# Kernel optimization log

Hardware: AMD Instinct MI355X
Metric: run time of the kernel (lower is better)

The kernel has to match this reference:

```python
import jax, jax.numpy as jnp
import numpy as np

PAD = 3            # pad_size
K = 3              # kernel_size
MAX_DISP = 20      # max_displacement
STRIDE1 = 1
STRIDE2 = 2

B, C, H, W = 4, 128, 192, 192


def _correlation(input1, input2):
    """FlowNetC/PWC-Net correlation cost volume (correlation_pwc semantics).

    input1, input2: [B, C, H, W]
    returns: [B, D*D, Hout, Wout] where D = 2*(MAX_DISP//STRIDE2)+1.
    """
    b, c, h, w = input1.shape
    kr = (K - 1) // 2                      # kernel radius
    br = kr + MAX_DISP                     # border radius
    hp, wp = h + 2 * PAD, w + 2 * PAD      # padded sizes
    hout = (hp - 2 * br) // STRIDE1
    wout = (wp - 2 * br) // STRIDE1
    gr = MAX_DISP // STRIDE2               # neighborhood grid radius
    disp = jnp.arange(-gr, gr + 1, dtype=jnp.int32) * STRIDE2
    # channel order: tj (dy) outer, ti (dx) inner, matching the CUDA kernel
    dyx = jnp.stack(jnp.meshgrid(disp, disp, indexing='ij'), axis=-1).reshape(-1, 2)

    pad1 = jnp.pad(input1, ((0, 0), (0, 0), (PAD, PAD), (PAD, PAD)))
    pad2 = jnp.pad(input2, ((0, 0), (0, 0), (PAD, PAD), (PAD, PAD)))

    # region of pad1 touched by all outputs (stride1 == 1)
    hh, ww = hout * STRIDE1 + 2 * kr, wout * STRIDE1 + 2 * kr
    s1 = pad1[:, :, MAX_DISP:MAX_DISP + hh, MAX_DISP:MAX_DISP + ww]
    nelems = K * K * c

    def step(_, d):
        dy, dx = d[0], d[1]
        s2 = jax.lax.dynamic_slice(pad2, (0, 0, MAX_DISP + dy, MAX_DISP + dx),
                                   (b, c, hh, ww))
        prod = jnp.sum(s1 * s2, axis=1)  # [B, hh, ww] reduce channels
        summed = jax.lax.reduce_window(prod, 0.0, jax.lax.add,
                                       (1, K, K), (1, STRIDE1, STRIDE1), 'VALID')
        return None, summed / nelems      # [B, Hout, Wout]

    _, out = jax.lax.scan(step, None, dyx)   # [D*D, B, Hout, Wout]
    return jnp.transpose(out, (1, 0, 2, 3))  # [B, D*D, Hout, Wout]


def setup_inputs() -> dict:
    key = jax.random.key(0)
    k1, k2 = jax.random.split(key)
    input1 = jax.random.normal(k1, (B, C, H, W), dtype=jnp.float32)
    input2 = jax.random.normal(k2, (B, C, H, W), dtype=jnp.float32)
    return {"input1": input1, "input2": input2}


def reference(input1, input2):
    return _correlation(input1, input2)
```

## Files before the change

### kernel.cpp

```cpp
#include <hip/hip_runtime.h>
#include <hip/hip_bf16.h>


#define C_    128
#define H_    192
#define W_    192
#define HW_   36864
#define NE_   18874368
#define CORR_E 44036496
#define WS_NEED 163570464ull

typedef __attribute__((ext_vector_type(8))) short short8;
typedef __attribute__((ext_vector_type(4))) float floatx4;

__device__ __forceinline__ float bf2f(ushort h) {
    uint u = ((uint)h) << 16;
    return __builtin_bit_cast(float, u);
}
__device__ __forceinline__ ushort f2bf(float f) {
    __hip_bfloat16 hb = __float2bfloat16(f);
    return *(ushort*)&hb;
}

__global__ __launch_bounds__(256)
void cvt_t_kernel(const float* __restrict__ a, const float* __restrict__ b,
                  ushort* __restrict__ dst0) {
    __shared__ float tile[128 * 65];
    const float* src = blockIdx.z ? b : a;
    ushort* dst = dst0 + (size_t)blockIdx.z * NE_;
    const int bb = blockIdx.y;
    const int hw0 = blockIdx.x * 64;
    const int t = threadIdx.x;
    const int xr = (t & 15) * 4;
    const int c0 = t >> 4;
    const float* sbase = src + (size_t)bb * C_ * HW_ + hw0;
#pragma unroll
    for (int pass = 0; pass < 8; ++pass) {
        const int c = c0 + 16 * pass;
        float4 v = *(const float4*)(sbase + (size_t)c * HW_ + xr);
        float* lp = &tile[c * 65 + xr];
        lp[0] = v.x; lp[1] = v.y; lp[2] = v.z; lp[3] = v.w;
    }
    __syncthreads();
    ushort* obase = dst + ((size_t)bb * HW_ + hw0) * 128;
#pragma unroll
    for (int pass = 0; pass < 4; ++pass) {
        const int u = t + 256 * pass;
        const int x = u >> 4, oc = u & 15;
        uint w[4];
#pragma unroll
        for (int k = 0; k < 4; ++k) {
            const float f0 = tile[(oc * 8 + 2 * k) * 65 + x];
            const float f1 = tile[(oc * 8 + 2 * k + 1) * 65 + x];
            w[k] = (uint)f2bf(f0) | ((uint)f2bf(f1) << 16);
        }
        uint4 o; o.x = w[0]; o.y = w[1]; o.z = w[2]; o.w = w[3];
        *(uint4*)(obase + (size_t)x * 128 + oc * 8) = o;
    }
}

__global__ __launch_bounds__(256, 6)
void corr_mfma(const ushort* __restrict__ in1t, const ushort* __restrict__ in2t,
               ushort* __restrict__ corrw) {
    __shared__ ushort ctile[2][1428];
    const int tid = threadIdx.x;
    const int j0 = blockIdx.x * 32;
    const int ytile = blockIdx.y;
    const int zz = blockIdx.z;
    const int b = zz >> 1, q = zz & 1;
    const int ybase = q + 4 * ytile;
    const int lane = tid & 63, wav = tid >> 6;
    const int yrow = wav >> 1, p = wav & 1;
    const int mn = lane & 15, quad = lane >> 4;

    const int arow = ybase + 2 * yrow + 17;
    const int ax = j0 + 17 + 2 * mn + p;
    const ushort* aptr = in1t + ((size_t)((b * H_ + arow) * W_ + ax)) * C_ + quad * 8;
    short8 afr[4];
#pragma unroll
    for (int kb = 0; kb < 4; ++kb) afr[kb] = *(const short8*)(aptr + kb * 32);

    const int ybY = ybase + 2 * yrow - 3;
    const ushort* bptr[3];
    bool colok[3];
#pragma unroll
    for (int u3 = 0; u3 < 3; ++u3) {
        const int xp = j0 - 3 + p + 2 * (u3 * 16 + mn);
        colok[u3] = ((unsigned)xp < (unsigned)W_);
        bptr[u3] = in2t + (ptrdiff_t)((b * H_ + ybY) * W_ + xp) * C_ + quad * 8;
    }

    const short8 z8 = {0, 0, 0, 0, 0, 0, 0, 0};
    const size_t planebase = (size_t)b * 441;

    for (int dyi = 0; dyi < 21; ++dyi) {
        floatx4 acc[3];
#pragma unroll
        for (int u3 = 0; u3 < 3; ++u3) acc[u3] = (floatx4){0.f, 0.f, 0.f, 0.f};
        const bool rowok = ((unsigned)(ybY + 2 * dyi) < (unsigned)H_);
        if (rowok) {
#pragma unroll
            for (int u3 = 0; u3 < 3; ++u3) {
                short8 b0 = z8, b1 = z8, b2 = z8, b3 = z8;
                if (colok[u3]) {
                    const ushort* bp = bptr[u3];
                    b0 = *(const short8*)(bp);
                    b1 = *(const short8*)(bp + 32);
                    b2 = *(const short8*)(bp + 64);
                    b3 = *(const short8*)(bp + 96);
                }
                acc[u3] = __builtin_amdgcn_mfma_f32_16x16x32_bf16(afr[0], b0, acc[u3], 0, 0, 0);
                acc[u3] = __builtin_amdgcn_mfma_f32_16x16x32_bf16(afr[1], b1, acc[u3], 0, 0, 0);
                acc[u3] = __builtin_amdgcn_mfma_f32_16x16x32_bf16(afr[2], b2, acc[u3], 0, 0, 0);
                acc[u3] = __builtin_amdgcn_mfma_f32_16x16x32_bf16(afr[3], b3, acc[u3], 0, 0, 0);
            }
        }
#pragma unroll
        for (int u3 = 0; u3 < 3; ++u3) bptr[u3] += 2 * W_ * C_;

        ushort* ct = &ctile[dyi & 1][0];
#pragma unroll
        for (int u3 = 0; u3 < 3; ++u3) {
#pragma unroll
            for (int v = 0; v < 4; ++v) {
                const int mr = quad * 4 + v;
                const int t = u3 * 16 + mn - mr;
                if (t >= 0 && t <= 20)
                    ct[t * 68 + yrow * 34 + 2 * mr + p] = f2bf(acc[u3][v]);
            }
        }
        __syncthreads();
#pragma unroll
        for (int it = 0; it < 3; ++it) {
            const int idx = tid + it * 256;
            if (idx < 672) {
                const int t = idx >> 5, rem = idx & 31;
                const int yy = rem >> 4, x2 = (rem & 15) << 1;
                const uint val = *(const uint*)(ct + t * 68 + yy * 34 + x2);
                const int Y = ybase + 2 * yy, X = j0 + x2;
                if (Y < 158 && X < 158) {
                    const size_t off = ((planebase + (size_t)(dyi * 21 + t)) * 158 + Y) * 158 + X;
                    *(uint*)(corrw + off) = val;
                }
            }
        }
    }
}

__global__ __launch_bounds__(256)
void window_kernel(const ushort* __restrict__ corrw, float* __restrict__ out) {
    __shared__ uint wsl[1440];
    const int tid = threadIdx.x;
    const int i0 = blockIdx.x * 16;
    const int plane = blockIdx.y;
    const ushort* cp = corrw + (size_t)plane * 24964;
    for (int task = tid; task < 1440; task += 256) {
        const int r = task / 80;
        const int dc = task - r * 80;
        const int row = i0 + r;
        if (dc < 79 && row < 158)
            wsl[task] = *(const uint*)(cp + row * 158 + dc * 2);
    }
    __syncthreads();
    if (tid < 156) {
        const ushort* cl = (const ushort*)wsl;
        float S[18];
#pragma unroll
        for (int r = 0; r < 18; ++r) {
            const ushort* rp = cl + r * 160 + tid;
            S[r] = bf2f(rp[0]) + bf2f(rp[1]) + bf2f(rp[2]);
        }
        const float sc = 1.f / 1152.f;
#pragma unroll
        for (int r = 0; r < 16; ++r) {
            const int row = i0 + r;
            if (row < 156)
                out[(size_t)plane * 24336 + (size_t)row * 156 + tid] =
                    (S[r] + S[r + 1] + S[r + 2]) * sc;
        }
    }
}

#define OUT_HW 156
#define NDISP 21
#define TILE_OUT 14
#define TILE_CORR 16
#define S2W 56
#define NT 256

__global__ __launch_bounds__(NT, 4)
void corr_fallback(const float* __restrict__ in1, const float* __restrict__ in2,
                   float* __restrict__ out) {
    __shared__ float s2s[TILE_CORR * S2W];
    __shared__ float corrs[NDISP * TILE_CORR * TILE_CORR];
    const int tid = threadIdx.x;
    const int tx = tid & 15;
    const int ty = tid >> 4;
    const int tj = blockIdx.x;
    const int ti = blockIdx.y;
    const int z = blockIdx.z;
    const int b = z / NDISP;
    const int dyi = z - b * NDISP;
    const int dy = 2 * dyi - 20;
    const int y0 = ti * TILE_OUT;
    const int x0 = tj * TILE_OUT;
    const int y = y0 + ty;
    const int x = x0 + tx;
    float acc[NDISP];
#pragma unroll
    for (int d = 0; d < NDISP; ++d) acc[d] = 0.f;
    const float* p1 = in1 + (size_t)b * C_ * HW_ + (size_t)(y + 17) * W_ + (x + 17);
    const float* p2base = in2 + (size_t)b * C_ * HW_;
    for (int c = 0; c < C_; ++c) {
        const float a = p1[(size_t)c * HW_];
        const float* p2 = p2base + (size_t)c * HW_;
        for (int idx = tid; idx < TILE_CORR * S2W; idx += NT) {
            const int r = idx / S2W;
            const int cc = idx - r * S2W;
            const int gr = y0 + r + 17 + dy;
            const int gc = x0 + cc - 3;
            float v = 0.f;
            if ((unsigned)gr < H_ && (unsigned)gc < W_) v = p2[gr * W_ + gc];
            s2s[idx] = v;
        }
        __syncthreads();
        const float* srow = &s2s[ty * S2W + tx];
#pragma unroll
        for (int d = 0; d < NDISP; ++d) acc[d] += a * srow[2 * d];
        __syncthreads();
    }
#pragma unroll
    for (int d = 0; d < NDISP; ++d)
        corrs[d * (TILE_CORR * TILE_CORR) + tid] = acc[d];
    __syncthreads();
    const float scale = 1.f / 1152.f;
    for (int o = tid; o < NDISP * TILE_OUT * TILE_OUT; o += NT) {
        const int d = o / (TILE_OUT * TILE_OUT);
        const int rem = o - d * (TILE_OUT * TILE_OUT);
        const int i = rem / TILE_OUT;
        const int j = rem - i * TILE_OUT;
        const float* cpt = &corrs[d * (TILE_CORR * TILE_CORR) + i * TILE_CORR + j];
        const float s = cpt[0] + cpt[1] + cpt[2]
                      + cpt[16] + cpt[17] + cpt[18]
                      + cpt[32] + cpt[33] + cpt[34];
        const int ig = y0 + i;
        const int jg = x0 + j;
        if (ig < OUT_HW && jg < OUT_HW) {
            const size_t oidx = (((size_t)b * (NDISP * NDISP) + (size_t)dyi * NDISP + d)
                                 * OUT_HW + ig) * OUT_HW + jg;
            out[oidx] = s * scale;
        }
    }
}

extern "C" void kernel_launch(void* const* d_in, const int* in_sizes, int n_in,
                              void* d_out, int out_size, void* d_ws, size_t ws_size,
                              hipStream_t stream) {
    const float* in1 = (const float*)d_in[0];
    const float* in2 = (const float*)d_in[1];
    float* out = (float*)d_out;

    if (ws_size >= WS_NEED) {
        ushort* wsp = (ushort*)d_ws;
        ushort* in1t = wsp;
        ushort* in2t = wsp + (size_t)NE_;
        ushort* corrw = wsp + (size_t)2 * NE_;
        cvt_t_kernel<<<dim3(576, 4, 2), 256, 0, stream>>>(in1, in2, wsp);
        corr_mfma<<<dim3(5, 40, 8), 256, 0, stream>>>(in1t, in2t, corrw);
        window_kernel<<<dim3(10, 1764), 256, 0, stream>>>(corrw, out);
    } else {
        corr_fallback<<<dim3(12, 12, 84), 256, 0, stream>>>(in1, in2, out);
    }
}
```

Before: 574.8 us.

## Process two output row pairs per wave in correlation MFMA kernel

Each wave now holds A fragments for two output rows spaced four apart and computes both per displacement row, halving the grid in y and doubling the output tile per block. The block index is linearised so that consecutive blocks vary batch and parity first, which is meant to improve L2 reuse of in2 rows. B loads for columns beyond the needed range are skipped via an s<=36 mask. The kernel does more MFMA work per load pass but uses more registers, with occupancy lowered from 6 to 4, and the LDS tile and store loop are widened to match.

New measurement: 506.6 us. 1.13x faster.

```diff
diff --git a/kernel.cpp b/kernel.cpp
--- a/kernel.cpp
+++ b/kernel.cpp
@@ -59,34 +59,40 @@
     }
 }
 
-__global__ __launch_bounds__(256, 6)
+__global__ __launch_bounds__(256, 4)
 void corr_mfma(const ushort* __restrict__ in1t, const ushort* __restrict__ in2t,
                ushort* __restrict__ corrw) {
-    __shared__ ushort ctile[2][1428];
+    __shared__ ushort ctile[2][21 * 136];
     const int tid = threadIdx.x;
-    const int j0 = blockIdx.x * 32;
-    const int ytile = blockIdx.y;
-    const int zz = blockIdx.z;
+    const int lin = blockIdx.x + 5 * (blockIdx.y + 20 * blockIdx.z);
+    const int zz = lin & 7;
+    const int rem = lin >> 3;
+    const int j0 = (rem % 5) * 32;
+    const int ytile = rem / 5;
     const int b = zz >> 1, q = zz & 1;
-    const int ybase = q + 4 * ytile;
+    const int ybase = q + 8 * ytile;
     const int lane = tid & 63, wav = tid >> 6;
     const int yrow = wav >> 1, p = wav & 1;
     const int mn = lane & 15, quad = lane >> 4;
 
-    const int arow = ybase + 2 * yrow + 17;
     const int ax = j0 + 17 + 2 * mn + p;
-    const ushort* aptr = in1t + ((size_t)((b * H_ + arow) * W_ + ax)) * C_ + quad * 8;
-    short8 afr[4];
-#pragma unroll
-    for (int kb = 0; kb < 4; ++kb) afr[kb] = *(const short8*)(aptr + kb * 32);
+    short8 afr[2][4];
+#pragma unroll
+    for (int a = 0; a < 2; ++a) {
+        const int arow = ybase + 2 * yrow + 4 * a + 17;
+        const ushort* aptr = in1t + ((size_t)((b * H_ + arow) * W_ + ax)) * C_ + quad * 8;
+#pragma unroll
+        for (int kb = 0; kb < 4; ++kb) afr[a][kb] = *(const short8*)(aptr + kb * 32);
+    }
 
     const int ybY = ybase + 2 * yrow - 3;
     const ushort* bptr[3];
     bool colok[3];
 #pragma unroll
     for (int u3 = 0; u3 < 3; ++u3) {
-        const int xp = j0 - 3 + p + 2 * (u3 * 16 + mn);
-        colok[u3] = ((unsigned)xp < (unsigned)W_);
+        const int s = u3 * 16 + mn;
+        const int xp = j0 - 3 + p + 2 * s;
+        colok[u3] = ((unsigned)xp < (unsigned)W_) && (s <= 36);
         bptr[u3] = in2t + (ptrdiff_t)((b * H_ + ybY) * W_ + xp) * C_ + quad * 8;
     }
 
@@ -94,50 +100,58 @@
     const size_t planebase = (size_t)b * 441;
 
     for (int dyi = 0; dyi < 21; ++dyi) {
-        floatx4 acc[3];
-#pragma unroll
-        for (int u3 = 0; u3 < 3; ++u3) acc[u3] = (floatx4){0.f, 0.f, 0.f, 0.f};
-        const bool rowok = ((unsigned)(ybY + 2 * dyi) < (unsigned)H_);
-        if (rowok) {
+        floatx4 acc[2][3];
+#pragma unroll
+        for (int a = 0; a < 2; ++a)
+#pragma unroll
+            for (int u3 = 0; u3 < 3; ++u3) acc[a][u3] = (floatx4){0.f, 0.f, 0.f, 0.f};
+#pragma unroll
+        for (int a = 0; a < 2; ++a) {
+            const int yb = ybY + 2 * dyi + 4 * a;
+            if ((unsigned)yb < (unsigned)H_) {
+                const ptrdiff_t roff = (ptrdiff_t)(2 * dyi + 4 * a) * W_ * C_;
+#pragma unroll
+                for (int u3 = 0; u3 < 3; ++u3) {
+                    short8 b0 = z8, b1 = z8, b2 = z8, b3 = z8;
+                    if (colok[u3]) {
+                        const ushort* bp = bptr[u3] + roff;
+                        b0 = *(const short8*)(bp);
+                        b1 = *(const short8*)(bp + 32);
+                        b2 = *(const short8*)(bp + 64);
+                        b3 = *(const short8*)(bp + 96);
+                    }
+                    acc[a][u3] = __builtin_amdgcn_mfma_f32_16x16x32_bf16(afr[a][0], b0, acc[a][u3], 0, 0, 0);
+                    acc[a][u3] = __builtin_amdgcn_mfma_f32_16x16x32_bf16(afr[a][1], b1, acc[a][u3], 0, 0, 0);
+                    acc[a][u3] = __builtin_amdgcn_mfma_f32_16x16x32_bf16(afr[a][2], b2, acc[a][u3], 0, 0, 0);
+                    acc[a][u3] = __builtin_amdgcn_mfma_f32_16x16x32_bf16(afr[a][3], b3, acc[a][u3], 0, 0, 0);
+                }
+            }
+        }
+
+        ushort* ct = &ctile[dyi & 1][0];
+#pragma unroll
+        for (int a = 0; a < 2; ++a) {
+            const int rr = yrow + 2 * a;
 #pragma unroll
             for (int u3 = 0; u3 < 3; ++u3) {
-                short8 b0 = z8, b1 = z8, b2 = z8, b3 = z8;
-                if (colok[u3]) {
-                    const ushort* bp = bptr[u3];
-                    b0 = *(const short8*)(bp);
-                    b1 = *(const short8*)(bp + 32);
-                    b2 = *(const short8*)(bp + 64);
-                    b3 = *(const short8*)(bp + 96);
+#pragma unroll
+                for (int v = 0; v < 4; ++v) {
+                    const int mr = quad * 4 + v;
+                    const int t = u3 * 16 + mn - mr;
+                    if (t >= 0 && t <= 20)
+                        ct[t * 136 + rr * 34 + 2 * mr + p] = f2bf(acc[a][u3][v]);
                 }
-                acc[u3] = __builtin_amdgcn_mfma_f32_16x16x32_bf16(afr[0], b0, acc[u3], 0, 0, 0);
-                acc[u3] = __builtin_amdgcn_mfma_f32_16x16x32_bf16(afr[1], b1, acc[u3], 0, 0, 0);
-                acc[u3] = __builtin_amdgcn_mfma_f32_16x16x32_bf16(afr[2], b2, acc[u3], 0, 0, 0);
-                acc[u3] = __builtin_amdgcn_mfma_f32_16x16x32_bf16(afr[3], b3, acc[u3], 0, 0, 0);
             }
         }
-#pragma unroll
-        for (int u3 = 0; u3 < 3; ++u3) bptr[u3] += 2 * W_ * C_;
-
-        ushort* ct = &ctile[dyi & 1][0];
-#pragma unroll
-        for (int u3 = 0; u3 < 3; ++u3) {
-#pragma unroll
-            for (int v = 0; v < 4; ++v) {
-                const int mr = quad * 4 + v;
-                const int t = u3 * 16 + mn - mr;
-                if (t >= 0 && t <= 20)
-                    ct[t * 68 + yrow * 34 + 2 * mr + p] = f2bf(acc[u3][v]);
-            }
-        }
         __syncthreads();
 #pragma unroll
-        for (int it = 0; it < 3; ++it) {
+        for (int it = 0; it < 6; ++it) {
             const int idx = tid + it * 256;
-            if (idx < 672) {
-                const int t = idx >> 5, rem = idx & 31;
-                const int yy = rem >> 4, x2 = (rem & 15) << 1;
-                const uint val = *(const uint*)(ct + t * 68 + yy * 34 + x2);
-                const int Y = ybase + 2 * yy, X = j0 + x2;
+            if (idx < 1344) {
+                const int t = idx >> 6, rem2 = idx & 63;
+                const int rr = rem2 >> 4, x2 = (rem2 & 15) << 1;
+                const uint val = *(const uint*)(ct + t * 136 + rr * 34 + x2);
+                const int Y = ybase + 2 * rr, X = j0 + x2;
                 if (Y < 158 && X < 158) {
                     const size_t off = ((planebase + (size_t)(dyi * 21 + t)) * 158 + Y) * 158 + X;
                     *(uint*)(corrw + off) = val;
@@ -266,7 +280,7 @@
         ushort* in2t = wsp + (size_t)NE_;
         ushort* corrw = wsp + (size_t)2 * NE_;
         cvt_t_kernel<<<dim3(576, 4, 2), 256, 0, stream>>>(in1, in2, wsp);
-        corr_mfma<<<dim3(5, 40, 8), 256, 0, stream>>>(in1t, in2t, corrw);
+        corr_mfma<<<dim3(5, 20, 8), 256, 0, stream>>>(in1t, in2t, corrw);
         window_kernel<<<dim3(10, 1764), 256, 0, stream>>>(corrw, out);
     } else {
         corr_fallback<<<dim3(12, 12, 84), 256, 0, stream>>>(in1, in2, out);
```
